# Kernel tuning notes

Hardware: AMD Instinct MI355X
Metric: run time of the kernel (lower is better)

Reference implementation:

```python
import jax, jax.numpy as jnp
import numpy as np

N, E0 = 50000, 800000          # nodes, raw edges (self-loops appended in reference)
IN, H, C = 128, 8, 8           # in_channels, heads, out_channels per head
ED, T = 16, 96                 # edge_dim, temporal profile length
NEG_SLOPE = 0.2                # leaky relu slope
CW = 0.5                       # complementarity_weight


def setup_inputs() -> dict:
    key = jax.random.key(0)
    ks = jax.random.split(key, 12)
    def xavier(k, shape):
        fan_in, fan_out = shape[1], shape[0]
        lim = np.sqrt(6.0 / (fan_in + fan_out)).astype(np.float32)
        return jax.random.uniform(k, shape, jnp.float32, -lim, lim)
    return {
        "x": jax.random.normal(ks[0], (N, IN), jnp.float32),
        "edge_index": jax.random.randint(ks[1], (2, E0), 0, N, jnp.int64),
        "edge_attr": jax.random.normal(ks[2], (E0, ED), jnp.float32),
        "temporal_profiles": jax.random.normal(ks[3], (N, T), jnp.float32),
        "Wq": xavier(ks[4], (H * C, IN)),
        "Wk": xavier(ks[5], (H * C, IN)),
        "Wv": xavier(ks[6], (H * C, IN)),
        "We": xavier(ks[7], (H * C, ED)),
        "comp_W": xavier(ks[8], (H, 2 * IN)),
        "comp_b": jnp.zeros((H,), jnp.float32),
        "Wo": xavier(ks[9], (C, H * C)),
        "bo": jnp.zeros((C,), jnp.float32),
    }


def reference(x, edge_index, edge_attr, temporal_profiles,
              Wq, Wk, Wv, We, comp_W, comp_b, Wo, bo):
    n = x.shape[0]
    # ---- add self loops (PyG add_self_loops; edge_attr filled with 1.0) ----
    loops = jnp.arange(n, dtype=edge_index.dtype)
    ei = jnp.concatenate([edge_index, jnp.stack([loops, loops])], axis=1)
    ea = jnp.concatenate(
        [edge_attr, jnp.ones((n, edge_attr.shape[1]), edge_attr.dtype)], axis=0)
    src, dst = ei[0], ei[1]  # key/value side (j) = src, query side (i) = dst

    # ---- node projections [N, H, C] ----
    q = (x @ Wq.T).reshape(n, H, C)
    k = (x @ Wk.T).reshape(n, H, C)
    v = (x @ Wv.T).reshape(n, H, C)

    # ---- complementarity scores per edge ----
    tp = temporal_profiles
    tpn = (tp - tp.mean(axis=1, keepdims=True)) / \
          (tp.std(axis=1, ddof=1, keepdims=True) + 1e-8)  # torch std is unbiased
    correlation = (tpn[src] * tpn[dst]).mean(axis=1)       # [E]
    # Linear(2*IN -> H) on concat([x[src], x[dst]]) == split matmul per node
    a_node = x @ comp_W[:, :IN].T                          # [N, H]
    b_node = x @ comp_W[:, IN:].T                          # [N, H]
    learned = jnp.tanh(a_node[src] + b_node[dst] + comp_b).mean(axis=1)
    comp = 0.5 * correlation + 0.5 * learned               # [E]

    # ---- per-edge attention logits ----
    key_j = k[src]                                         # [E, H, C]
    alpha = (q[dst] * key_j).sum(-1) / np.sqrt(C).astype(np.float32)  # [E, H]
    edge_feat = (ea @ We.T).reshape(-1, H, C)
    alpha = alpha + (edge_feat * key_j).sum(-1)
    alpha = alpha + CW * (-comp)[:, None]
    alpha = jnp.where(alpha >= 0, alpha, NEG_SLOPE * alpha)  # leaky_relu

    # ---- segment softmax over destination nodes (PyG softmax) ----
    amax = jax.ops.segment_max(alpha, dst, num_segments=n)   # every node has a self loop
    e = jnp.exp(alpha - amax[dst])
    denom = jax.ops.segment_sum(e, dst, num_segments=n)
    att = e / (denom[dst] + 1e-16)                           # [E, H]

    # ---- weighted scatter-add aggregation ----
    msg = v[src] * att[:, :, None]                           # [E, H, C]
    out = jax.ops.segment_sum(msg, dst, num_segments=n).reshape(n, H * C)
    return out @ Wo.T + bo
```

## Files before the change

### kernel.cpp

```cpp
#include <hip/hip_runtime.h>
#include <math.h>


struct __align__(8) US4 { unsigned short x, y, z, w; };

typedef __attribute__((ext_vector_type(8))) short bf16x8;
typedef __attribute__((ext_vector_type(4))) float f32x4;

#define CH 32

__device__ __forceinline__ unsigned short f2bf(float f) {
    unsigned u = __float_as_uint(f);
    unsigned r = (u + 0x7fffu + ((u >> 16) & 1u)) >> 16;
    return (unsigned short)r;
}
__device__ __forceinline__ float bf2f(unsigned short u) {
    return __uint_as_float(((unsigned)u) << 16);
}
__device__ __forceinline__ float blo(unsigned u) { return __uint_as_float(u << 16); }
__device__ __forceinline__ float bhi(unsigned u) { return __uint_as_float(u & 0xffff0000u); }

__global__ __launch_bounds__(256) void k_bpack(
    const float* __restrict__ Wq, const float* __restrict__ Wk, const float* __restrict__ Wv,
    const float* __restrict__ compW, const float* __restrict__ We,
    unsigned short* __restrict__ Bp)
{
    int gid = blockIdx.x * 256 + threadIdx.x;
    if (gid >= 21 * 2048) return;
    int i = gid & 7, lane = (gid >> 3) & 63, s = (gid >> 9) & 3, t = gid >> 11;
    int col = t * 16 + (lane & 15);
    int k = s * 32 + ((lane >> 4) << 3) + i;
    float v;
    if (col < 64)        v = Wq[col * 128 + k];
    else if (col < 128)  v = Wk[(col - 64) * 128 + k];
    else if (col < 192)  v = Wv[(col - 128) * 128 + k];
    else if (col < 200)  v = compW[(col - 192) * 256 + k];
    else if (col < 208)  v = compW[(col - 200) * 256 + 128 + k];
    else {
        int hd = col - 208, h = hd >> 4, d = hd & 15;
        v = 0.f;
        #pragma unroll
        for (int c = 0; c < 8; c++)
            v += Wk[(h * 8 + c) * 128 + k] * We[(h * 8 + c) * 16 + d];
    }
    Bp[gid] = f2bf(v);
}

__device__ __forceinline__ bf16x8 ld_bf8(const float* p) {
    float4 a = ((const float4*)p)[0], b = ((const float4*)p)[1];
    bf16x8 r;
    r[0] = (short)f2bf(a.x); r[1] = (short)f2bf(a.y);
    r[2] = (short)f2bf(a.z); r[3] = (short)f2bf(a.w);
    r[4] = (short)f2bf(b.x); r[5] = (short)f2bf(b.y);
    r[6] = (short)f2bf(b.z); r[7] = (short)f2bf(b.w);
    return r;
}

__global__ __launch_bounds__(256) void k_gemm(
    const float* __restrict__ x, const unsigned short* __restrict__ Bp,
    const float* __restrict__ compb,
    float* __restrict__ q, unsigned short* __restrict__ rec, int N)
{
    const int tid = threadIdx.x, w = tid >> 6, lane = tid & 63;
    const int half = lane >> 4;
    const int c0 = lane & 15;
    int row_a = blockIdx.x * 64 + w * 16 + c0;
    int ra = min(row_a, N - 1);
    const float* xr = x + (size_t)ra * 128 + half * 8;
    bf16x8 a0 = ld_bf8(xr +  0);
    bf16x8 a1 = ld_bf8(xr + 32);
    bf16x8 a2 = ld_bf8(xr + 64);
    bf16x8 a3 = ld_bf8(xr + 96);
    const int rbase = blockIdx.x * 64 + w * 16 + half * 4;
    const float cbv = compb[c0 & 7];

    for (int t = 0; t < 21; t++) {
        f32x4 acc = {0.f, 0.f, 0.f, 0.f};
        const bf16x8* bp = (const bf16x8*)(Bp + (size_t)((t * 4) * 64 + lane) * 8);
        acc = __builtin_amdgcn_mfma_f32_16x16x32_bf16(a0, bp[0],   acc, 0, 0, 0);
        acc = __builtin_amdgcn_mfma_f32_16x16x32_bf16(a1, bp[64],  acc, 0, 0, 0);
        acc = __builtin_amdgcn_mfma_f32_16x16x32_bf16(a2, bp[128], acc, 0, 0, 0);
        acc = __builtin_amdgcn_mfma_f32_16x16x32_bf16(a3, bp[192], acc, 0, 0, 0);
        #pragma unroll
        for (int r = 0; r < 4; r++) {
            int rr = rbase + r;
            if (rr >= N) continue;
            float vr = acc[r];
            unsigned short* recR = rec + (size_t)rr * 384;
            if (t < 4)        q[(size_t)rr * 64 + t * 16 + c0] = vr * 0.35355339059327373f;
            else if (t < 8)   recR[(t - 4) * 16 + c0] = f2bf(vr);
            else if (t < 12)  recR[192 + (t - 8) * 16 + c0] = f2bf(vr);
            else if (t == 12) {
                if (c0 < 8) ((float*)(recR + 352))[c0] = vr;
                else        ((float*)(recR + 368))[c0 - 8] = vr + cbv;
            }
            else              recR[64 + (t - 13) * 16 + c0] = f2bf(vr);
        }
    }
}

__global__ __launch_bounds__(256) void k_tpn(const float* __restrict__ tp,
                                             unsigned short* __restrict__ rec, int N)
{
    int wave = threadIdx.x >> 6;
    int lane = threadIdx.x & 63;
    int n = blockIdx.x * 4 + wave;
    if (n >= N) return;
    const float* row = tp + (size_t)n * 96;
    float v0 = row[lane];
    float v1 = (lane < 32) ? row[64 + lane] : 0.f;
    float s = v0 + v1, ss = v0 * v0 + v1 * v1;
    #pragma unroll
    for (int m = 1; m < 64; m <<= 1) { s += __shfl_xor(s, m); ss += __shfl_xor(ss, m); }
    float mean = s * (1.f / 96.f);
    float var = (ss - 96.f * mean * mean) * (1.f / 95.f);
    var = fmaxf(var, 0.f);
    float inv = 1.f / (sqrtf(var) + 1e-8f);
    unsigned short* orow = rec + (size_t)n * 384 + 256;
    orow[lane] = f2bf((v0 - mean) * inv);
    if (lane < 32) orow[64 + lane] = f2bf((v1 - mean) * inv);
}

__global__ __launch_bounds__(256) void k_hist(const int* __restrict__ ei,
                                              int* __restrict__ deg,
                                              int* __restrict__ rnk, int E0, int N)
{
    int e = blockIdx.x * 256 + threadIdx.x;
    int E = E0 + N;
    if (e >= E) return;
    int dst = (e < E0) ? ei[E0 + e] : (e - E0);
    rnk[e] = atomicAdd(&deg[dst], 1);
}

__global__ __launch_bounds__(256) void k_scanA(const int* __restrict__ deg,
                                               int* __restrict__ bsum, int N)
{
    __shared__ int sm[256];
    int i = blockIdx.x * 256 + threadIdx.x;
    sm[threadIdx.x] = (i < N) ? deg[i] : 0;
    __syncthreads();
    for (int off = 128; off > 0; off >>= 1) {
        if (threadIdx.x < off) sm[threadIdx.x] += sm[threadIdx.x + off];
        __syncthreads();
    }
    if (threadIdx.x == 0) bsum[blockIdx.x] = sm[0];
}

__global__ __launch_bounds__(256) void k_scanB(int* __restrict__ bsum, int NB)
{
    __shared__ int sm[256];
    int t = threadIdx.x;
    sm[t] = (t < NB) ? bsum[t] : 0;
    __syncthreads();
    for (int off = 1; off < 256; off <<= 1) {
        int v = (t >= off) ? sm[t - off] : 0;
        __syncthreads();
        sm[t] += v;
        __syncthreads();
    }
    if (t < NB) bsum[t] = (t == 0) ? 0 : sm[t - 1];
}

__global__ __launch_bounds__(256) void k_scanC(const int* __restrict__ deg,
                                               const int* __restrict__ bsum,
                                               int* __restrict__ row, int N)
{
    __shared__ int sm[256];
    int b = blockIdx.x, t = threadIdx.x, i = b * 256 + t;
    int v = (i < N) ? deg[i] : 0;
    sm[t] = v;
    __syncthreads();
    for (int off = 1; off < 256; off <<= 1) {
        int u = (t >= off) ? sm[t - off] : 0;
        __syncthreads();
        sm[t] += u;
        __syncthreads();
    }
    int excl = bsum[b] + sm[t] - v;
    if (i < N) {
        row[i] = excl;
        if (i == N - 1) row[N] = excl + v;
    }
}

__global__ __launch_bounds__(256) void k_scatter(const int* __restrict__ ei,
                                                 const int* __restrict__ row,
                                                 const int* __restrict__ rnk,
                                                 int2* __restrict__ csrd, int E0, int N)
{
    int e = blockIdx.x * 256 + threadIdx.x;
    int E = E0 + N;
    if (e >= E) return;
    int src, dst;
    if (e < E0) { src = ei[e]; dst = ei[E0 + e]; }
    else        { src = e - E0; dst = src; }
    int pos = row[dst] + rnk[e];
    csrd[pos] = make_int2(e, src);
}

__global__ __launch_bounds__(256) void k_nodeattn(
    const int2* __restrict__ csrd, const int* __restrict__ row,
    const float* __restrict__ eattr,
    const float* __restrict__ q, const unsigned short* __restrict__ rec,
    const float* __restrict__ Wo, const float* __restrict__ bo,
    float* __restrict__ out, int E0, int N)
{
    const int tid = threadIdx.x;
    const int wave = tid >> 6, lane = tid & 63;
    const int n = blockIdx.x * 4 + wave;
    if (n >= N) return;

    const int beg = row[n], end = row[n + 1];
    const int h = lane & 7;
    const int g = lane >> 3;
    const int koff = h * 8;
    const int goff = 64 + h * 16;
    const int voff = 192 + h * 8;
    const int toff = 256 + h * 12;

    const unsigned short* recN = rec + (size_t)n * 384;
    const float4* qp = (const float4*)(q + (size_t)n * 64 + h * 8);
    const float4 qd0 = qp[0], qd1 = qp[1];
    const uint2* tdp = (const uint2*)(recN + toff);
    const uint2 td0 = tdp[0], td1 = tdp[1], td2 = tdp[2];
    const float bnh = ((const float*)(recN + 368))[h];

    float m_reg = -1e30f, dsum = 0.f;
    float acc[8];
    #pragma unroll
    for (int c = 0; c < 8; c++) acc[c] = 0.f;

    for (int cbeg = beg; cbeg < end; cbeg += CH) {
        const int cnt = min(CH, end - cbeg);

        float av[4];
        uint4 vu[4];
        #pragma unroll
        for (int j = 0; j < 4; j++) {
            av[j] = -1e30f;
            vu[j] = make_uint4(0u, 0u, 0u, 0u);
            int eo = g + 8 * j;
            if (eo < cnt) {
                int2 es = csrd[cbeg + eo];
                const int e = es.x, s = es.y;
                const unsigned short* recS = rec + (size_t)s * 384;

                vu[j] = *(const uint4*)(recS + voff);

                const US4* kp = (const US4*)(recS + koff);
                US4 k0 = kp[0], k1 = kp[1];
                float qk = qd0.x*bf2f(k0.x) + qd0.y*bf2f(k0.y) + qd0.z*bf2f(k0.z) + qd0.w*bf2f(k0.w)
                         + qd1.x*bf2f(k1.x) + qd1.y*bf2f(k1.y) + qd1.z*bf2f(k1.z) + qd1.w*bf2f(k1.w);

                const uint4* gp = (const uint4*)(recS + goff);
                uint4 g0 = gp[0], g1 = gp[1];
                int ec = (e < E0) ? e : 0;
                const float4* ep4 = (const float4*)(eattr + (size_t)ec * 16);
                float4 e0 = ep4[0], e1 = ep4[1], e2 = ep4[2], e3 = ep4[3];
                if (e >= E0) {
                    e0 = make_float4(1.f, 1.f, 1.f, 1.f); e1 = e0; e2 = e0; e3 = e0;
                }
                float efk = e0.x*blo(g0.x) + e0.y*bhi(g0.x) + e0.z*blo(g0.y) + e0.w*bhi(g0.y)
                          + e1.x*blo(g0.z) + e1.y*bhi(g0.z) + e1.z*blo(g0.w) + e1.w*bhi(g0.w)
                          + e2.x*blo(g1.x) + e2.y*bhi(g1.x) + e2.z*blo(g1.y) + e2.w*bhi(g1.y)
                          + e3.x*blo(g1.z) + e3.y*bhi(g1.z) + e3.z*blo(g1.w) + e3.w*bhi(g1.w);

                float tv = ((const float*)(recS + 352))[h] + bnh;
                float ex = __expf(2.f * tv);
                float tn = 1.f - 2.f / (ex + 1.f);

                const uint2* tsp = (const uint2*)(recS + toff);
                uint2 s0 = tsp[0], s1 = tsp[1], s2 = tsp[2];
                float pc = blo(s0.x)*blo(td0.x) + bhi(s0.x)*bhi(td0.x)
                         + blo(s0.y)*blo(td0.y) + bhi(s0.y)*bhi(td0.y)
                         + blo(s1.x)*blo(td1.x) + bhi(s1.x)*bhi(td1.x)
                         + blo(s1.y)*blo(td1.y) + bhi(s1.y)*bhi(td1.y)
                         + blo(s2.x)*blo(td2.x) + bhi(s2.x)*bhi(td2.x)
                         + blo(s2.y)*blo(td2.y) + bhi(s2.y)*bhi(td2.y);
                float cv = pc * (-0.25f / 96.f) + tn * (-0.25f / 8.f);
                cv += __shfl_xor(cv, 1); cv += __shfl_xor(cv, 2); cv += __shfl_xor(cv, 4);

                float a = qk + efk + cv;
                av[j] = fmaxf(a, 0.2f * a);
            }
        }

        float mloc = fmaxf(fmaxf(av[0], av[1]), fmaxf(av[2], av[3]));
        mloc = fmaxf(mloc, __shfl_xor(mloc, 8));
        mloc = fmaxf(mloc, __shfl_xor(mloc, 16));
        mloc = fmaxf(mloc, __shfl_xor(mloc, 32));

        float mn = fmaxf(m_reg, mloc);
        float sc = __expf(m_reg - mn);
        m_reg = mn;
        dsum *= sc;
        #pragma unroll
        for (int c = 0; c < 8; c++) acc[c] *= sc;

        #pragma unroll
        for (int j = 0; j < 4; j++) {
            float p = __expf(av[j] - mn);
            dsum += p;
            acc[0] += p * blo(vu[j].x); acc[1] += p * bhi(vu[j].x);
            acc[2] += p * blo(vu[j].y); acc[3] += p * bhi(vu[j].y);
            acc[4] += p * blo(vu[j].z); acc[5] += p * bhi(vu[j].z);
            acc[6] += p * blo(vu[j].w); acc[7] += p * bhi(vu[j].w);
        }
    }

    dsum += __shfl_xor(dsum, 8); dsum += __shfl_xor(dsum, 16); dsum += __shfl_xor(dsum, 32);
    #pragma unroll
    for (int c = 0; c < 8; c++) {
        acc[c] += __shfl_xor(acc[c], 8);
        acc[c] += __shfl_xor(acc[c], 16);
        acc[c] += __shfl_xor(acc[c], 32);
    }
    float inv = 1.f / (dsum + 1e-16f);

    float po[8];
    #pragma unroll
    for (int cp8 = 0; cp8 < 8; cp8++) {
        const float4* wr = (const float4*)(Wo + cp8 * 64 + h * 8);
        float4 w0 = wr[0], w1 = wr[1];
        po[cp8] = inv * (acc[0]*w0.x + acc[1]*w0.y + acc[2]*w0.z + acc[3]*w0.w
                       + acc[4]*w1.x + acc[5]*w1.y + acc[6]*w1.z + acc[7]*w1.w);
    }
    #pragma unroll
    for (int cp8 = 0; cp8 < 8; cp8++) {
        po[cp8] += __shfl_xor(po[cp8], 1);
        po[cp8] += __shfl_xor(po[cp8], 2);
        po[cp8] += __shfl_xor(po[cp8], 4);
    }
    if (lane < 8) out[(size_t)n * 8 + lane] = po[lane] + bo[lane];
}

extern "C" void kernel_launch(void* const* d_in, const int* in_sizes, int n_in,
                              void* d_out, int out_size, void* d_ws, size_t ws_size,
                              hipStream_t stream)
{
    const float* x     = (const float*)d_in[0];
    const int*   ei    = (const int*)d_in[1];
    const float* eattr = (const float*)d_in[2];
    const float* tp    = (const float*)d_in[3];
    const float* Wq    = (const float*)d_in[4];
    const float* Wk    = (const float*)d_in[5];
    const float* Wv    = (const float*)d_in[6];
    const float* We    = (const float*)d_in[7];
    const float* compW = (const float*)d_in[8];
    const float* compb = (const float*)d_in[9];
    const float* Wo    = (const float*)d_in[10];
    const float* bo    = (const float*)d_in[11];
    float* out = (float*)d_out;

    const int N  = in_sizes[0] / 128;
    const int E0 = in_sizes[1] / 2;
    const int E  = E0 + N;
    const int NB = (N + 255) / 256;

    float* ws = (float*)d_ws;
    size_t off = 0;
    unsigned short* rec = (unsigned short*)(ws + off); off += (size_t)N * 192;
    float* q  = ws + off; off += (size_t)N * 64;
    int* deg    = (int*)(ws + off); off += N;
    int* bsum   = (int*)(ws + off); off += 256;
    int* rowp   = (int*)(ws + off); off += N + 4;
    unsigned short* Bp = (unsigned short*)(ws + off); off += 21504;
    int2* csrd  = (int2*)(ws + off); off += (size_t)E * 2;
    int* rnk    = (int*)(ws + off); off += E;

    hipMemsetAsync(deg, 0, (size_t)N * sizeof(int), stream);

    k_hist<<<(E + 255) / 256, 256, 0, stream>>>(ei, deg, rnk, E0, N);
    k_scanA<<<NB, 256, 0, stream>>>(deg, bsum, N);
    k_scanB<<<1, 256, 0, stream>>>(bsum, NB);
    k_scanC<<<NB, 256, 0, stream>>>(deg, bsum, rowp, N);
    k_scatter<<<(E + 255) / 256, 256, 0, stream>>>(ei, rowp, rnk, csrd, E0, N);

    k_bpack<<<(21 * 2048 + 255) / 256, 256, 0, stream>>>(Wq, Wk, Wv, compW, We, Bp);
    k_gemm<<<(N + 63) / 64, 256, 0, stream>>>(x, Bp, compb, q, rec, N);
    k_tpn<<<(N + 3) / 4, 256, 0, stream>>>(tp, rec, N);

    k_nodeattn<<<(N + 3) / 4, 256, 0, stream>>>(csrd, rowp, eattr, q, rec,
                                                Wo, bo, out, E0, N);
}
```

Baseline: 219.7 us.

## Quantize normalized temporal profiles to int8 and shrink per-node record

Stores the normalized temporal profiles as int8 (scale 12, clamped to ±127) instead of bf16, and moves the destination-only b_node term out of the gathered per-node record into a separate array. The record shrinks from 768 to 640 bytes, which cuts the bytes fetched for each random source gather in the edge attention loop. The destination profile is dequantized once per node into registers with the scale folded in. The cost is extra unpack work per edge and coarser correlation precision, including clipping of values beyond about 10.6 standard deviations.

```diff
diff --git a/kernel.cpp b/kernel.cpp
--- a/kernel.cpp
+++ b/kernel.cpp
@@ -59,7 +59,8 @@
 __global__ __launch_bounds__(256) void k_gemm(
     const float* __restrict__ x, const unsigned short* __restrict__ Bp,
     const float* __restrict__ compb,
-    float* __restrict__ q, unsigned short* __restrict__ rec, int N)
+    float* __restrict__ q, unsigned short* __restrict__ rec,
+    float* __restrict__ bnArr, int N)
 {
     const int tid = threadIdx.x, w = tid >> 6, lane = tid & 63;
     const int half = lane >> 4;
@@ -86,13 +87,13 @@
             int rr = rbase + r;
             if (rr >= N) continue;
             float vr = acc[r];
-            unsigned short* recR = rec + (size_t)rr * 384;
+            unsigned short* recR = rec + (size_t)rr * 320;
             if (t < 4)        q[(size_t)rr * 64 + t * 16 + c0] = vr * 0.35355339059327373f;
             else if (t < 8)   recR[(t - 4) * 16 + c0] = f2bf(vr);
             else if (t < 12)  recR[192 + (t - 8) * 16 + c0] = f2bf(vr);
             else if (t == 12) {
-                if (c0 < 8) ((float*)(recR + 352))[c0] = vr;
-                else        ((float*)(recR + 368))[c0 - 8] = vr + cbv;
+                if (c0 < 8) ((float*)(recR + 304))[c0] = vr;
+                else        bnArr[(size_t)rr * 8 + (c0 - 8)] = vr + cbv;
             }
             else              recR[64 + (t - 13) * 16 + c0] = f2bf(vr);
         }
@@ -115,10 +116,16 @@
     float mean = s * (1.f / 96.f);
     float var = (ss - 96.f * mean * mean) * (1.f / 95.f);
     var = fmaxf(var, 0.f);
-    float inv = 1.f / (sqrtf(var) + 1e-8f);
-    unsigned short* orow = rec + (size_t)n * 384 + 256;
-    orow[lane] = f2bf((v0 - mean) * inv);
-    if (lane < 32) orow[64 + lane] = f2bf((v1 - mean) * inv);
+    float inv = 12.f / (sqrtf(var) + 1e-8f);
+    if (lane < 24) {
+        float4 v = ((const float4*)row)[lane];
+        int q0 = (int)rintf(fminf(fmaxf((v.x - mean) * inv, -127.f), 127.f));
+        int q1 = (int)rintf(fminf(fmaxf((v.y - mean) * inv, -127.f), 127.f));
+        int q2 = (int)rintf(fminf(fmaxf((v.z - mean) * inv, -127.f), 127.f));
+        int q3 = (int)rintf(fminf(fmaxf((v.w - mean) * inv, -127.f), 127.f));
+        unsigned pk = (q0 & 255) | ((q1 & 255) << 8) | ((q2 & 255) << 16) | ((q3 & 255) << 24);
+        *((unsigned*)(rec + (size_t)n * 320 + 256) + lane) = pk;
+    }
 }
 
 __global__ __launch_bounds__(256) void k_hist(const int* __restrict__ ei,
@@ -202,6 +209,7 @@
     const int2* __restrict__ csrd, const int* __restrict__ row,
     const float* __restrict__ eattr,
     const float* __restrict__ q, const unsigned short* __restrict__ rec,
+    const float* __restrict__ bnArr,
     const float* __restrict__ Wo, const float* __restrict__ bo,
     float* __restrict__ out, int E0, int N)
 {
@@ -216,14 +224,23 @@
     const int koff = h * 8;
     const int goff = 64 + h * 16;
     const int voff = 192 + h * 8;
-    const int toff = 256 + h * 12;
-
-    const unsigned short* recN = rec + (size_t)n * 384;
+
+    const unsigned short* recN = rec + (size_t)n * 320;
     const float4* qp = (const float4*)(q + (size_t)n * 64 + h * 8);
     const float4 qd0 = qp[0], qd1 = qp[1];
-    const uint2* tdp = (const uint2*)(recN + toff);
-    const uint2 td0 = tdp[0], td1 = tdp[1], td2 = tdp[2];
-    const float bnh = ((const float*)(recN + 368))[h];
+    const float bnh = bnArr[(size_t)n * 8 + h];
+    float tdf[12];
+    {
+        const unsigned* tdq = (const unsigned*)(recN + 256) + h * 3;
+        unsigned w0 = tdq[0], w1 = tdq[1], w2 = tdq[2];
+        const float CC = -0.25f / (96.f * 144.f);
+        tdf[0] = (float)((int)(w0 << 24) >> 24) * CC; tdf[1] = (float)((int)(w0 << 16) >> 24) * CC;
+        tdf[2] = (float)((int)(w0 <<  8) >> 24) * CC; tdf[3] = (float)((int)w0 >> 24) * CC;
+        tdf[4] = (float)((int)(w1 << 24) >> 24) * CC; tdf[5] = (float)((int)(w1 << 16) >> 24) * CC;
+        tdf[6] = (float)((int)(w1 <<  8) >> 24) * CC; tdf[7] = (float)((int)w1 >> 24) * CC;
+        tdf[8] = (float)((int)(w2 << 24) >> 24) * CC; tdf[9] = (float)((int)(w2 << 16) >> 24) * CC;
+        tdf[10] = (float)((int)(w2 << 8) >> 24) * CC; tdf[11] = (float)((int)w2 >> 24) * CC;
+    }
 
     float m_reg = -1e30f, dsum = 0.f;
     float acc[8];
@@ -243,7 +260,7 @@
             if (eo < cnt) {
                 int2 es = csrd[cbeg + eo];
                 const int e = es.x, s = es.y;
-                const unsigned short* recS = rec + (size_t)s * 384;
+                const unsigned short* recS = rec + (size_t)s * 320;
 
                 vu[j] = *(const uint4*)(recS + voff);
 
@@ -265,19 +282,20 @@
                           + e2.x*blo(g1.x) + e2.y*bhi(g1.x) + e2.z*blo(g1.y) + e2.w*bhi(g1.y)
                           + e3.x*blo(g1.z) + e3.y*bhi(g1.z) + e3.z*blo(g1.w) + e3.w*bhi(g1.w);
 
-                float tv = ((const float*)(recS + 352))[h] + bnh;
+                float tv = ((const float*)(recS + 304))[h] + bnh;
                 float ex = __expf(2.f * tv);
                 float tn = 1.f - 2.f / (ex + 1.f);
 
-                const uint2* tsp = (const uint2*)(recS + toff);
-                uint2 s0 = tsp[0], s1 = tsp[1], s2 = tsp[2];
-                float pc = blo(s0.x)*blo(td0.x) + bhi(s0.x)*bhi(td0.x)
-                         + blo(s0.y)*blo(td0.y) + bhi(s0.y)*bhi(td0.y)
-                         + blo(s1.x)*blo(td1.x) + bhi(s1.x)*bhi(td1.x)
-                         + blo(s1.y)*blo(td1.y) + bhi(s1.y)*bhi(td1.y)
-                         + blo(s2.x)*blo(td2.x) + bhi(s2.x)*bhi(td2.x)
-                         + blo(s2.y)*blo(td2.y) + bhi(s2.y)*bhi(td2.y);
-                float cv = pc * (-0.25f / 96.f) + tn * (-0.25f / 8.f);
+                const unsigned* tsq = (const unsigned*)(recS + 256) + h * 3;
+                unsigned x0 = tsq[0], x1 = tsq[1], x2 = tsq[2];
+                float pc =
+                    (float)((int)(x0 << 24) >> 24) * tdf[0] + (float)((int)(x0 << 16) >> 24) * tdf[1]
+                  + (float)((int)(x0 <<  8) >> 24) * tdf[2] + (float)((int)x0 >> 24) * tdf[3]
+                  + (float)((int)(x1 << 24) >> 24) * tdf[4] + (float)((int)(x1 << 16) >> 24) * tdf[5]
+                  + (float)((int)(x1 <<  8) >> 24) * tdf[6] + (float)((int)x1 >> 24) * tdf[7]
+                  + (float)((int)(x2 << 24) >> 24) * tdf[8] + (float)((int)(x2 << 16) >> 24) * tdf[9]
+                  + (float)((int)(x2 <<  8) >> 24) * tdf[10] + (float)((int)x2 >> 24) * tdf[11];
+                float cv = pc + tn * (-0.25f / 8.f);
                 cv += __shfl_xor(cv, 1); cv += __shfl_xor(cv, 2); cv += __shfl_xor(cv, 4);
 
                 float a = qk + efk + cv;
@@ -359,8 +377,9 @@
 
     float* ws = (float*)d_ws;
     size_t off = 0;
-    unsigned short* rec = (unsigned short*)(ws + off); off += (size_t)N * 192;
+    unsigned short* rec = (unsigned short*)(ws + off); off += (size_t)N * 160;
     float* q  = ws + off; off += (size_t)N * 64;
+    float* bnArr = ws + off; off += (size_t)N * 8;
     int* deg    = (int*)(ws + off); off += N;
     int* bsum   = (int*)(ws + off); off += 256;
     int* rowp   = (int*)(ws + off); off += N + 4;
@@ -377,9 +396,9 @@
     k_scatter<<<(E + 255) / 256, 256, 0, stream>>>(ei, rowp, rnk, csrd, E0, N);
 
     k_bpack<<<(21 * 2048 + 255) / 256, 256, 0, stream>>>(Wq, Wk, Wv, compW, We, Bp);
-    k_gemm<<<(N + 63) / 64, 256, 0, stream>>>(x, Bp, compb, q, rec, N);
+    k_gemm<<<(N + 63) / 64, 256, 0, stream>>>(x, Bp, compb, q, rec, bnArr, N);
     k_tpn<<<(N + 3) / 4, 256, 0, stream>>>(tp, rec, N);
 
-    k_nodeattn<<<(N + 3) / 4, 256, 0, stream>>>(csrd, rowp, eattr, q, rec,
+    k_nodeattn<<<(N + 3) / 4, 256, 0, stream>>>(csrd, rowp, eattr, q, rec, bnArr,
                                                 Wo, bo, out, E0, N);
 }
```

Result: faster. 207.2 us (-5.7%).
